# Kernel optimization log

Measured on AMD Instinct MI355X. Metric: run time of the kernel, lower is better.

The kernel has to match this reference:

```python
import jax, jax.numpy as jnp
import numpy as np

N = 100000       # nodes
DEG = 16         # in-degree per node
E = N * DEG      # edges
IN_DIM = 128
H_DIM = 128
NEG_SLOPE = 0.01  # F.leaky_relu default


def setup_inputs() -> dict:
    key = jax.random.key(0)
    ks = jax.random.split(key, 12)
    sc = 0.05
    attr = jax.random.normal(ks[0], (N, IN_DIM), jnp.float32)
    edge_d = jax.random.uniform(ks[1], (E, 1), dtype=jnp.float32)
    edge_src = jax.random.randint(ks[2], (E,), 0, N, dtype=jnp.int32)
    edge_dst = jnp.repeat(jnp.arange(N, dtype=jnp.int32), DEG)  # every node gets DEG msgs
    return {
        "attr": attr,
        "edge_d": edge_d,
        "W_V1": jax.random.normal(ks[3], (1, 1), jnp.float32) * sc,
        "W_W1": jax.random.normal(ks[4], (H_DIM, IN_DIM), jnp.float32) * sc,
        "W_U1": jax.random.normal(ks[5], (H_DIM, IN_DIM), jnp.float32) * sc,
        "W_a1": jax.random.normal(ks[6], (1, 2 * H_DIM + 1), jnp.float32) * sc,
        "W_V2": jax.random.normal(ks[7], (1, 1), jnp.float32) * sc,
        "W_W2": jax.random.normal(ks[8], (H_DIM, H_DIM), jnp.float32) * sc,
        "W_U2": jax.random.normal(ks[9], (H_DIM, H_DIM), jnp.float32) * sc,
        "W_a2": jax.random.normal(ks[10], (1, 2 * H_DIM + 1), jnp.float32) * sc,
        "edge_src": edge_src,
        "edge_dst": edge_dst,
    }


def gat_layer(h, edge_d, edge_src, edge_dst, W_V, W_W, W_U, W_a):
    n = h.shape[0]
    t = edge_d @ W_V.T                      # [E,1] edge feature transform (fcV)
    z = h @ W_W.T                           # [N,H] (fcW)
    z_i = h @ W_U.T                         # [N,H] (fcU)
    Hd = z.shape[1]
    a = W_a[0]                              # [2H+1]
    a_src, a_dst, a_t = a[:Hd], a[Hd:2 * Hd], a[2 * Hd:]
    # attn_fc(concat(z_src, z_dst, t)) decomposed into per-node scores + edge term
    s_src = z @ a_src                       # [N]
    s_dst = z @ a_dst                       # [N]
    e = s_src[edge_src] + s_dst[edge_dst] + (t @ a_t)  # [E]
    e = jax.nn.leaky_relu(e, NEG_SLOPE)
    # per-destination-node softmax over incoming edges (mailbox softmax)
    m = jax.ops.segment_max(e, edge_dst, num_segments=n)
    ex = jnp.exp(e - m[edge_dst])
    denom = jax.ops.segment_sum(ex, edge_dst, num_segments=n)
    alpha = ex / denom[edge_dst]            # [E]
    # weighted neighbor aggregation
    zn = jax.ops.segment_sum(alpha[:, None] * z[edge_src], edge_dst, num_segments=n)
    return jax.nn.relu(z_i + zn)


def reference(attr, edge_d, W_V1, W_W1, W_U1, W_a1, W_V2, W_W2, W_U2, W_a2,
              edge_src, edge_dst):
    h = gat_layer(attr, edge_d, edge_src, edge_dst, W_V1, W_W1, W_U1, W_a1)
    h = gat_layer(h, edge_d, edge_src, edge_dst, W_V2, W_W2, W_U2, W_a2)
    return h
```

## Files before the change

kernel.cpp:

```cpp
#include <hip/hip_runtime.h>

#define N_NODES 100000
#define DEG 16
#define DIM 128
#define NGROUPS 6250
#define GPB 2
#define DBLOCKS (NGROUPS / GPB)

typedef short bf16x8 __attribute__((ext_vector_type(8)));
typedef float f32x4 __attribute__((ext_vector_type(4)));

__device__ __forceinline__ unsigned short f2bf(float f) {
    unsigned int u = __builtin_bit_cast(unsigned int, f);
    u = (u + 0x7fffu + ((u >> 16) & 1u)) >> 16;
    return (unsigned short)u;
}
__device__ __forceinline__ float bf2f(unsigned short h) {
    unsigned int u = ((unsigned int)h) << 16;
    return __builtin_bit_cast(float, u);
}
__device__ __forceinline__ bf16x8 pack_bf16x8(float4 lo, float4 hi) {
    bf16x8 f;
    f[0] = (short)f2bf(lo.x); f[1] = (short)f2bf(lo.y);
    f[2] = (short)f2bf(lo.z); f[3] = (short)f2bf(lo.w);
    f[4] = (short)f2bf(hi.x); f[5] = (short)f2bf(hi.y);
    f[6] = (short)f2bf(hi.z); f[7] = (short)f2bf(hi.w);
    return f;
}

template <bool F32IN>
__global__ __launch_bounds__(256, 2) void dense_fused(
    const void* __restrict__ hsrc,
    const float* __restrict__ W_W,
    const float* __restrict__ W_U,
    const float* __restrict__ W_a,
    unsigned short* __restrict__ zcat,
    float* __restrict__ s_src0, float* __restrict__ s_src1,
    float* __restrict__ s_dst0, float* __restrict__ s_dst1)
{
    const int wave = threadIdx.x >> 6;
    const int lane = threadIdx.x & 63;
    const int n16 = lane & 15;
    const int quad = lane >> 4;
    const int gbase = blockIdx.x * GPB;

    float4 hraw[GPB][8];
    bf16x8 hfrag[GPB][4];
#pragma unroll
    for (int g = 0; g < GPB; g++) {
        int nodebase = (gbase + g) * 16;
        if constexpr (F32IN) {
            const float* hrow = (const float*)hsrc + (size_t)(nodebase + n16) * DIM + quad * 8;
#pragma unroll
            for (int ks = 0; ks < 4; ks++) {
                hraw[g][ks * 2]     = *(const float4*)(hrow + ks * 32);
                hraw[g][ks * 2 + 1] = *(const float4*)(hrow + ks * 32 + 4);
            }
        } else {
            const unsigned short* hrow = (const unsigned short*)hsrc + (size_t)(nodebase + n16) * DIM + quad * 8;
#pragma unroll
            for (int ks = 0; ks < 4; ks++)
                hfrag[g][ks] = *(const bf16x8*)(hrow + ks * 32);
        }
    }

    const float* Wbase = (wave < 2) ? (W_W + (size_t)wave * 64 * DIM)
                                    : (W_U + (size_t)(wave - 2) * 64 * DIM);
    bf16x8 wfrag[4][4];
#pragma unroll
    for (int half = 0; half < 2; half++) {
        float4 wraw[2][4][2];
#pragma unroll
        for (int c = 0; c < 2; c++) {
            int ct = half * 2 + c;
            const float* wrow = Wbase + (size_t)(ct * 16 + n16) * DIM + quad * 8;
#pragma unroll
            for (int ks = 0; ks < 4; ks++) {
                wraw[c][ks][0] = *(const float4*)(wrow + ks * 32);
                wraw[c][ks][1] = *(const float4*)(wrow + ks * 32 + 4);
            }
        }
#pragma unroll
        for (int c = 0; c < 2; c++)
#pragma unroll
            for (int ks = 0; ks < 4; ks++)
                wfrag[half * 2 + c][ks] = pack_bf16x8(wraw[c][ks][0], wraw[c][ks][1]);
    }

    if constexpr (F32IN) {
#pragma unroll
        for (int g = 0; g < GPB; g++)
#pragma unroll
            for (int ks = 0; ks < 4; ks++)
                hfrag[g][ks] = pack_bf16x8(hraw[g][ks * 2], hraw[g][ks * 2 + 1]);
    }

#pragma unroll
    for (int g = 0; g < GPB; g++) {
        const int nodebase = (gbase + g) * 16;

        f32x4 acc[4];
#pragma unroll
        for (int ct = 0; ct < 4; ct++) {
            f32x4 a = {0.f, 0.f, 0.f, 0.f};
#pragma unroll
            for (int ks = 0; ks < 4; ks++)
                a = __builtin_amdgcn_mfma_f32_16x16x32_bf16(wfrag[ct][ks], hfrag[g][ks], a, 0, 0, 0);
            acc[ct] = a;
        }

        unsigned short* orow = zcat + (size_t)(nodebase + n16) * 256 + wave * 64 + quad * 4;
#pragma unroll
        for (int ct = 0; ct < 4; ct++) {
            uint2 pk;
            pk.x = (unsigned int)f2bf(acc[ct][0]) | ((unsigned int)f2bf(acc[ct][1]) << 16);
            pk.y = (unsigned int)f2bf(acc[ct][2]) | ((unsigned int)f2bf(acc[ct][3]) << 16);
            *(uint2*)(orow + ct * 16) = pk;
        }

        if (wave < 2) {
            float ps = 0.f, pd = 0.f;
#pragma unroll
            for (int ct = 0; ct < 4; ct++) {
                float4 as = *(const float4*)(W_a + wave * 64 + ct * 16 + quad * 4);
                float4 ad = *(const float4*)(W_a + DIM + wave * 64 + ct * 16 + quad * 4);
                ps += acc[ct][0] * as.x + acc[ct][1] * as.y
                    + acc[ct][2] * as.z + acc[ct][3] * as.w;
                pd += acc[ct][0] * ad.x + acc[ct][1] * ad.y
                    + acc[ct][2] * ad.z + acc[ct][3] * ad.w;
            }
            ps += __shfl_xor(ps, 16); ps += __shfl_xor(ps, 32);
            pd += __shfl_xor(pd, 16); pd += __shfl_xor(pd, 32);
            if (lane < 16) {
                float* sp = wave == 0 ? s_src0 : s_src1;
                float* dp = wave == 0 ? s_dst0 : s_dst1;
                sp[nodebase + lane] = ps;
                dp[nodebase + lane] = pd;
            }
        }
    }
}

__global__ __launch_bounds__(256, 3) void aggr_kernel(
    const unsigned short* __restrict__ zcat,
    const float* __restrict__ s_src0, const float* __restrict__ s_src1,
    const float* __restrict__ s_dst0, const float* __restrict__ s_dst1,
    const float* __restrict__ edge_d,
    const int* __restrict__ edge_src,
    const float* __restrict__ W_V,
    const float* __restrict__ W_a,
    unsigned short* __restrict__ out_bf16,
    float* __restrict__ out_f32)
{
    __shared__ float alpha_s[16][DEG];
    __shared__ int   src_s[16][DEG];

    const int t = threadIdx.x;
    const int base = blockIdx.x * 16;

    {
        int nl = t >> 4, j = t & 15;
        int node = base + nl;
        int e = node * DEG + j;
        int s = edge_src[e];
        float coef = W_V[0] * W_a[2 * DIM];
        float x = (s_src0[s] + s_src1[s]) + (s_dst0[node] + s_dst1[node])
                + edge_d[e] * coef;
        x = x > 0.f ? x : 0.01f * x;
        float m = x;
        m = fmaxf(m, __shfl_xor(m, 1));
        m = fmaxf(m, __shfl_xor(m, 2));
        m = fmaxf(m, __shfl_xor(m, 4));
        m = fmaxf(m, __shfl_xor(m, 8));
        float ex = __expf(x - m);
        float d = ex;
        d += __shfl_xor(d, 1); d += __shfl_xor(d, 2);
        d += __shfl_xor(d, 4); d += __shfl_xor(d, 8);
        alpha_s[nl][j] = ex / d;
        src_s[nl][j] = s;
    }
    __syncthreads();

    const int nl = t >> 4;
    const int node = base + nl;
    const int c8 = (t & 15) * 8;

    uint4 raw[DEG];
#pragma unroll
    for (int j = 0; j < DEG; j++)
        raw[j] = *(const uint4*)(zcat + (size_t)src_s[nl][j] * 256 + c8);
    uint4 zr = *(const uint4*)(zcat + (size_t)node * 256 + 128 + c8);

    float acc[8] = {};
#pragma unroll
    for (int j = 0; j < DEG; j++) {
        float a = alpha_s[nl][j];
        acc[0] += a * bf2f((unsigned short)raw[j].x);
        acc[1] += a * bf2f((unsigned short)(raw[j].x >> 16));
        acc[2] += a * bf2f((unsigned short)raw[j].y);
        acc[3] += a * bf2f((unsigned short)(raw[j].y >> 16));
        acc[4] += a * bf2f((unsigned short)raw[j].z);
        acc[5] += a * bf2f((unsigned short)(raw[j].z >> 16));
        acc[6] += a * bf2f((unsigned short)raw[j].w);
        acc[7] += a * bf2f((unsigned short)(raw[j].w >> 16));
    }

    float v[8];
    v[0] = fmaxf(bf2f((unsigned short)zr.x) + acc[0], 0.f);
    v[1] = fmaxf(bf2f((unsigned short)(zr.x >> 16)) + acc[1], 0.f);
    v[2] = fmaxf(bf2f((unsigned short)zr.y) + acc[2], 0.f);
    v[3] = fmaxf(bf2f((unsigned short)(zr.y >> 16)) + acc[3], 0.f);
    v[4] = fmaxf(bf2f((unsigned short)zr.z) + acc[4], 0.f);
    v[5] = fmaxf(bf2f((unsigned short)(zr.z >> 16)) + acc[5], 0.f);
    v[6] = fmaxf(bf2f((unsigned short)zr.w) + acc[6], 0.f);
    v[7] = fmaxf(bf2f((unsigned short)(zr.w >> 16)) + acc[7], 0.f);

    if (out_f32) {
        float* op = out_f32 + (size_t)node * DIM + c8;
        *(float4*)op       = make_float4(v[0], v[1], v[2], v[3]);
        *(float4*)(op + 4) = make_float4(v[4], v[5], v[6], v[7]);
    } else {
        uint4 pk;
        pk.x = (unsigned int)f2bf(v[0]) | ((unsigned int)f2bf(v[1]) << 16);
        pk.y = (unsigned int)f2bf(v[2]) | ((unsigned int)f2bf(v[3]) << 16);
        pk.z = (unsigned int)f2bf(v[4]) | ((unsigned int)f2bf(v[5]) << 16);
        pk.w = (unsigned int)f2bf(v[6]) | ((unsigned int)f2bf(v[7]) << 16);
        *(uint4*)(out_bf16 + (size_t)node * DIM + c8) = pk;
    }
}

extern "C" void kernel_launch(void* const* d_in, const int* in_sizes, int n_in,
                              void* d_out, int out_size, void* d_ws, size_t ws_size,
                              hipStream_t stream) {
    const float* attr     = (const float*)d_in[0];
    const float* edge_d   = (const float*)d_in[1];
    const float* W_V1     = (const float*)d_in[2];
    const float* W_W1     = (const float*)d_in[3];
    const float* W_U1     = (const float*)d_in[4];
    const float* W_a1     = (const float*)d_in[5];
    const float* W_V2     = (const float*)d_in[6];
    const float* W_W2     = (const float*)d_in[7];
    const float* W_U2     = (const float*)d_in[8];
    const float* W_a2     = (const float*)d_in[9];
    const int*   edge_src = (const int*)d_in[10];

    float* out = (float*)d_out;

    char* ws = (char*)d_ws;
    unsigned short* zcat = (unsigned short*)ws;
    unsigned short* h1   = (unsigned short*)(ws + 52u * 1024 * 1024);
    float* s_src0        = (float*)(ws + 78u * 1024 * 1024);
    float* s_src1        = (float*)(ws + 79u * 1024 * 1024);
    float* s_dst0        = (float*)(ws + 80u * 1024 * 1024);
    float* s_dst1        = (float*)(ws + 81u * 1024 * 1024);

    dense_fused<true><<<DBLOCKS, 256, 0, stream>>>(attr, W_W1, W_U1, W_a1, zcat,
                                                   s_src0, s_src1, s_dst0, s_dst1);
    aggr_kernel<<<NGROUPS, 256, 0, stream>>>(zcat, s_src0, s_src1, s_dst0, s_dst1,
                                             edge_d, edge_src, W_V1, W_a1, h1, nullptr);

    dense_fused<false><<<DBLOCKS, 256, 0, stream>>>(h1, W_W2, W_U2, W_a2, zcat,
                                                    s_src0, s_src1, s_dst0, s_dst1);
    aggr_kernel<<<NGROUPS, 256, 0, stream>>>(zcat, s_src0, s_src1, s_dst0, s_dst1,
                                             edge_d, edge_src, W_V2, W_a2, nullptr, out);
}
```

Measured before the change: 387.6 us.

## Tile dense GEMM through LDS and split z/z_i into separate buffers

Rewrites the dense projection kernel to stage a 64-row weight slice and a 64-node input tile in LDS, using a 2D grid over column-block (W or U half) and node tile. Previously each block loaded all 256 weight rows into registers for only 32 nodes. It also splits the interleaved zcat buffer into separate z and z_i arrays of stride 128. The neighbor gathers in aggregation then read a compact 256-byte row instead of a 512-byte strided one. The trade-offs are that the input tile is now read four times (once per column block) and the kernel depends on shared memory.

```diff
diff --git a/kernel.cpp b/kernel.cpp
--- a/kernel.cpp
+++ b/kernel.cpp
@@ -3,9 +3,8 @@
 #define N_NODES 100000
 #define DEG 16
 #define DIM 128
-#define NGROUPS 6250
-#define GPB 2
-#define DBLOCKS (NGROUPS / GPB)
+#define NTILES 1563
+#define LSTR 136
 
 typedef short bf16x8 __attribute__((ext_vector_type(8)));
 typedef float f32x4 __attribute__((ext_vector_type(4)));
@@ -29,87 +28,93 @@
 }
 
 template <bool F32IN>
-__global__ __launch_bounds__(256, 2) void dense_fused(
+__global__ __launch_bounds__(256, 4) void dense_tile(
     const void* __restrict__ hsrc,
     const float* __restrict__ W_W,
     const float* __restrict__ W_U,
     const float* __restrict__ W_a,
-    unsigned short* __restrict__ zcat,
+    unsigned short* __restrict__ z,
+    unsigned short* __restrict__ zi,
     float* __restrict__ s_src0, float* __restrict__ s_src1,
     float* __restrict__ s_dst0, float* __restrict__ s_dst1)
 {
-    const int wave = threadIdx.x >> 6;
-    const int lane = threadIdx.x & 63;
+    __shared__ unsigned short Wt[64 * LSTR];
+    __shared__ unsigned short Ht[64 * LSTR];
+
+    const int cb = blockIdx.x;
+    const int nodebase = blockIdx.y * 64;
+    const int t = threadIdx.x;
+
+    {
+        const float* Wsrc = (cb < 2 ? W_W : W_U) + (size_t)(cb & 1) * 64 * DIM;
+        int r = t >> 2, c0 = (t & 3) * 32;
+        const float* src = Wsrc + (size_t)r * DIM + c0;
+        float4 v[8];
+#pragma unroll
+        for (int i = 0; i < 8; i++) v[i] = *(const float4*)(src + i * 4);
+        unsigned short* dst = Wt + r * LSTR + c0;
+#pragma unroll
+        for (int i = 0; i < 4; i++)
+            *(bf16x8*)(dst + i * 8) = pack_bf16x8(v[2 * i], v[2 * i + 1]);
+    }
+    {
+        int r = t >> 2, c0 = (t & 3) * 32;
+        int node = nodebase + r;
+        unsigned short* dst = Ht + r * LSTR + c0;
+        if (F32IN) {
+            float4 v[8];
+#pragma unroll
+            for (int i = 0; i < 8; i++) v[i] = make_float4(0.f, 0.f, 0.f, 0.f);
+            if (node < N_NODES) {
+                const float* src = (const float*)hsrc + (size_t)node * DIM + c0;
+#pragma unroll
+                for (int i = 0; i < 8; i++) v[i] = *(const float4*)(src + i * 4);
+            }
+#pragma unroll
+            for (int i = 0; i < 4; i++)
+                *(bf16x8*)(dst + i * 8) = pack_bf16x8(v[2 * i], v[2 * i + 1]);
+        } else {
+            uint4 u[4];
+#pragma unroll
+            for (int i = 0; i < 4; i++) u[i] = make_uint4(0, 0, 0, 0);
+            if (node < N_NODES) {
+                const unsigned short* src = (const unsigned short*)hsrc + (size_t)node * DIM + c0;
+#pragma unroll
+                for (int i = 0; i < 4; i++) u[i] = *(const uint4*)(src + i * 8);
+            }
+#pragma unroll
+            for (int i = 0; i < 4; i++) *(uint4*)(dst + i * 8) = u[i];
+        }
+    }
+    __syncthreads();
+
+    const int wave = t >> 6;
+    const int lane = t & 63;
     const int n16 = lane & 15;
     const int quad = lane >> 4;
-    const int gbase = blockIdx.x * GPB;
-
-    float4 hraw[GPB][8];
-    bf16x8 hfrag[GPB][4];
-#pragma unroll
-    for (int g = 0; g < GPB; g++) {
-        int nodebase = (gbase + g) * 16;
-        if constexpr (F32IN) {
-            const float* hrow = (const float*)hsrc + (size_t)(nodebase + n16) * DIM + quad * 8;
-#pragma unroll
-            for (int ks = 0; ks < 4; ks++) {
-                hraw[g][ks * 2]     = *(const float4*)(hrow + ks * 32);
-                hraw[g][ks * 2 + 1] = *(const float4*)(hrow + ks * 32 + 4);
-            }
-        } else {
-            const unsigned short* hrow = (const unsigned short*)hsrc + (size_t)(nodebase + n16) * DIM + quad * 8;
-#pragma unroll
-            for (int ks = 0; ks < 4; ks++)
-                hfrag[g][ks] = *(const bf16x8*)(hrow + ks * 32);
-        }
-    }
-
-    const float* Wbase = (wave < 2) ? (W_W + (size_t)wave * 64 * DIM)
-                                    : (W_U + (size_t)(wave - 2) * 64 * DIM);
-    bf16x8 wfrag[4][4];
-#pragma unroll
-    for (int half = 0; half < 2; half++) {
-        float4 wraw[2][4][2];
-#pragma unroll
-        for (int c = 0; c < 2; c++) {
-            int ct = half * 2 + c;
-            const float* wrow = Wbase + (size_t)(ct * 16 + n16) * DIM + quad * 8;
-#pragma unroll
-            for (int ks = 0; ks < 4; ks++) {
-                wraw[c][ks][0] = *(const float4*)(wrow + ks * 32);
-                wraw[c][ks][1] = *(const float4*)(wrow + ks * 32 + 4);
-            }
-        }
-#pragma unroll
-        for (int c = 0; c < 2; c++)
-#pragma unroll
-            for (int ks = 0; ks < 4; ks++)
-                wfrag[half * 2 + c][ks] = pack_bf16x8(wraw[c][ks][0], wraw[c][ks][1]);
-    }
-
-    if constexpr (F32IN) {
-#pragma unroll
-        for (int g = 0; g < GPB; g++)
-#pragma unroll
-            for (int ks = 0; ks < 4; ks++)
-                hfrag[g][ks] = pack_bf16x8(hraw[g][ks * 2], hraw[g][ks * 2 + 1]);
-    }
-
-#pragma unroll
-    for (int g = 0; g < GPB; g++) {
-        const int nodebase = (gbase + g) * 16;
-
-        f32x4 acc[4];
-#pragma unroll
-        for (int ct = 0; ct < 4; ct++) {
-            f32x4 a = {0.f, 0.f, 0.f, 0.f};
-#pragma unroll
-            for (int ks = 0; ks < 4; ks++)
-                a = __builtin_amdgcn_mfma_f32_16x16x32_bf16(wfrag[ct][ks], hfrag[g][ks], a, 0, 0, 0);
-            acc[ct] = a;
-        }
-
-        unsigned short* orow = zcat + (size_t)(nodebase + n16) * 256 + wave * 64 + quad * 4;
+    const int node = nodebase + wave * 16 + n16;
+
+    bf16x8 hfrag[4];
+    const unsigned short* hrow = Ht + (wave * 16 + n16) * LSTR + quad * 8;
+#pragma unroll
+    for (int ks = 0; ks < 4; ks++)
+        hfrag[ks] = *(const bf16x8*)(hrow + ks * 32);
+
+    f32x4 acc[4];
+#pragma unroll
+    for (int ct = 0; ct < 4; ct++) {
+        const unsigned short* wrow = Wt + (ct * 16 + n16) * LSTR + quad * 8;
+        f32x4 a = {0.f, 0.f, 0.f, 0.f};
+#pragma unroll
+        for (int ks = 0; ks < 4; ks++)
+            a = __builtin_amdgcn_mfma_f32_16x16x32_bf16(
+                    *(const bf16x8*)(wrow + ks * 32), hfrag[ks], a, 0, 0, 0);
+        acc[ct] = a;
+    }
+
+    if (node < N_NODES) {
+        unsigned short* zout = (cb < 2 ? z : zi);
+        unsigned short* orow = zout + (size_t)node * DIM + (cb & 1) * 64 + quad * 4;
 #pragma unroll
         for (int ct = 0; ct < 4; ct++) {
             uint2 pk;
@@ -117,32 +122,31 @@
             pk.y = (unsigned int)f2bf(acc[ct][2]) | ((unsigned int)f2bf(acc[ct][3]) << 16);
             *(uint2*)(orow + ct * 16) = pk;
         }
-
-        if (wave < 2) {
-            float ps = 0.f, pd = 0.f;
-#pragma unroll
-            for (int ct = 0; ct < 4; ct++) {
-                float4 as = *(const float4*)(W_a + wave * 64 + ct * 16 + quad * 4);
-                float4 ad = *(const float4*)(W_a + DIM + wave * 64 + ct * 16 + quad * 4);
-                ps += acc[ct][0] * as.x + acc[ct][1] * as.y
-                    + acc[ct][2] * as.z + acc[ct][3] * as.w;
-                pd += acc[ct][0] * ad.x + acc[ct][1] * ad.y
-                    + acc[ct][2] * ad.z + acc[ct][3] * ad.w;
-            }
-            ps += __shfl_xor(ps, 16); ps += __shfl_xor(ps, 32);
-            pd += __shfl_xor(pd, 16); pd += __shfl_xor(pd, 32);
-            if (lane < 16) {
-                float* sp = wave == 0 ? s_src0 : s_src1;
-                float* dp = wave == 0 ? s_dst0 : s_dst1;
-                sp[nodebase + lane] = ps;
-                dp[nodebase + lane] = pd;
-            }
+    }
+
+    if (cb < 2) {
+        float ps = 0.f, pd = 0.f;
+#pragma unroll
+        for (int ct = 0; ct < 4; ct++) {
+            float4 as = *(const float4*)(W_a + cb * 64 + ct * 16 + quad * 4);
+            float4 ad = *(const float4*)(W_a + DIM + cb * 64 + ct * 16 + quad * 4);
+            ps += acc[ct][0] * as.x + acc[ct][1] * as.y
+                + acc[ct][2] * as.z + acc[ct][3] * as.w;
+            pd += acc[ct][0] * ad.x + acc[ct][1] * ad.y
+                + acc[ct][2] * ad.z + acc[ct][3] * ad.w;
+        }
+        ps += __shfl_xor(ps, 16); ps += __shfl_xor(ps, 32);
+        pd += __shfl_xor(pd, 16); pd += __shfl_xor(pd, 32);
+        if (lane < 16 && node < N_NODES) {
+            (cb == 0 ? s_src0 : s_src1)[node] = ps;
+            (cb == 0 ? s_dst0 : s_dst1)[node] = pd;
         }
     }
 }
 
 __global__ __launch_bounds__(256, 3) void aggr_kernel(
-    const unsigned short* __restrict__ zcat,
+    const unsigned short* __restrict__ z,
+    const unsigned short* __restrict__ zi,
     const float* __restrict__ s_src0, const float* __restrict__ s_src1,
     const float* __restrict__ s_dst0, const float* __restrict__ s_dst1,
     const float* __restrict__ edge_d,
@@ -188,8 +192,8 @@
     uint4 raw[DEG];
 #pragma unroll
     for (int j = 0; j < DEG; j++)
-        raw[j] = *(const uint4*)(zcat + (size_t)src_s[nl][j] * 256 + c8);
-    uint4 zr = *(const uint4*)(zcat + (size_t)node * 256 + 128 + c8);
+        raw[j] = *(const uint4*)(z + (size_t)src_s[nl][j] * DIM + c8);
+    uint4 zr = *(const uint4*)(zi + (size_t)node * DIM + c8);
 
     float acc[8] = {};
 #pragma unroll
@@ -247,20 +251,23 @@
     float* out = (float*)d_out;
 
     char* ws = (char*)d_ws;
-    unsigned short* zcat = (unsigned short*)ws;
+    unsigned short* z    = (unsigned short*)ws;
+    unsigned short* zi   = (unsigned short*)(ws + 26u * 1024 * 1024);
     unsigned short* h1   = (unsigned short*)(ws + 52u * 1024 * 1024);
     float* s_src0        = (float*)(ws + 78u * 1024 * 1024);
     float* s_src1        = (float*)(ws + 79u * 1024 * 1024);
     float* s_dst0        = (float*)(ws + 80u * 1024 * 1024);
     float* s_dst1        = (float*)(ws + 81u * 1024 * 1024);
 
-    dense_fused<true><<<DBLOCKS, 256, 0, stream>>>(attr, W_W1, W_U1, W_a1, zcat,
-                                                   s_src0, s_src1, s_dst0, s_dst1);
-    aggr_kernel<<<NGROUPS, 256, 0, stream>>>(zcat, s_src0, s_src1, s_dst0, s_dst1,
-                                             edge_d, edge_src, W_V1, W_a1, h1, nullptr);
-
-    dense_fused<false><<<DBLOCKS, 256, 0, stream>>>(h1, W_W2, W_U2, W_a2, zcat,
-                                                    s_src0, s_src1, s_dst0, s_dst1);
-    aggr_kernel<<<NGROUPS, 256, 0, stream>>>(zcat, s_src0, s_src1, s_dst0, s_dst1,
-                                             edge_d, edge_src, W_V2, W_a2, nullptr, out);
-}
+    dim3 dgrid(4, NTILES);
+
+    dense_tile<true><<<dgrid, 256, 0, stream>>>(attr, W_W1, W_U1, W_a1, z, zi,
+                                                s_src0, s_src1, s_dst0, s_dst1);
+    aggr_kernel<<<6250, 256, 0, stream>>>(z, zi, s_src0, s_src1, s_dst0, s_dst1,
+                                          edge_d, edge_src, W_V1, W_a1, h1, nullptr);
+
+    dense_tile<false><<<dgrid, 256, 0, stream>>>(h1, W_W2, W_U2, W_a2, z, zi,
+                                                 s_src0, s_src1, s_dst0, s_dst1);
+    aggr_kernel<<<6250, 256, 0, stream>>>(z, zi, s_src0, s_src1, s_dst0, s_dst1,
+                                          edge_d, edge_src, W_V2, W_a2, nullptr, out);
+}
```

Result: faster. 350.0 us (-9.7%).
